# Kernel tuning notes

Measured on AMD Instinct MI355X. Metric: run time of the kernel, lower is better.

Reference implementation:

```python
import jax, jax.numpy as jnp
import numpy as np

B = 32        # num graphs
N = 512       # nodes per graph (equal-sized blocks)
HID = 512     # hidden_dim
H = 8         # num_heads
E = 262144    # num edges
ED = 16       # edge feature dim


def setup_inputs() -> dict:
    key = jax.random.key(0)
    ks = jax.random.split(key, 12)
    x = jax.random.normal(ks[0], (B * N, HID), jnp.float32)
    # contiguous, sorted graph assignment (equal-sized graphs)
    batch = jnp.repeat(jnp.arange(B, dtype=jnp.int64), N)
    # within-graph random edges
    g = jax.random.randint(ks[1], (E,), 0, B)
    src = g * N + jax.random.randint(ks[2], (E,), 0, N)
    dst = g * N + jax.random.randint(ks[3], (E,), 0, N)
    edge_index = jnp.stack([src, dst]).astype(jnp.int64)
    edge_attr = jax.random.normal(ks[4], (E, ED), jnp.float32)
    s = 1.0 / np.sqrt(HID).astype(np.float32)
    Wq = jax.random.normal(ks[5], (HID, HID), jnp.float32) * s
    Wk = jax.random.normal(ks[6], (HID, HID), jnp.float32) * s
    Wv = jax.random.normal(ks[7], (HID, HID), jnp.float32) * s
    Wo = jax.random.normal(ks[8], (HID, HID), jnp.float32) * s
    We = jax.random.normal(ks[9], (ED, H), jnp.float32) * (1.0 / np.sqrt(ED).astype(np.float32))
    bq = jnp.zeros((HID,), jnp.float32)
    bk = jnp.zeros((HID,), jnp.float32)
    bv = jnp.zeros((HID,), jnp.float32)
    bo = jnp.zeros((HID,), jnp.float32)
    be = jnp.zeros((H,), jnp.float32)
    return dict(x=x, batch=batch, edge_index=edge_index, edge_attr=edge_attr,
                Wq=Wq, bq=bq, Wk=Wk, bk=bk, Wv=Wv, bv=bv, Wo=Wo, bo=bo,
                We=We, be=be, num_graphs=B)


def reference(x, batch, edge_index, edge_attr, Wq, bq, Wk, bk, Wv, bv, Wo, bo, We, be, num_graphs):
    n_total, hid = x.shape
    n = n_total // num_graphs           # nodes per graph (equal blocks)
    hd = hid // H                       # head_dim
    scale = 1.0 / jnp.sqrt(jnp.asarray(hd, x.dtype))
    q = (x @ Wq + bq).reshape(num_graphs, n, H, hd)
    k = (x @ Wk + bk).reshape(num_graphs, n, H, hd)
    v = (x @ Wv + bv).reshape(num_graphs, n, H, hd)
    # per-graph dense scores: [B, n(query), m(key), H]
    attn = jnp.einsum('bnhd,bmhd->bnmh', q, k) * scale
    # edge-bias scatter-add (edges are intra-graph; local coords via div/mod)
    eb = edge_attr @ We + be                      # [E, H]
    b_idx = edge_index[0] // n
    loc_src = edge_index[0] % n
    loc_dst = edge_index[1] % n
    attn = attn.at[b_idx, loc_src, loc_dst].add(eb)
    # softmax over key axis (torch dim=1 of 'nmh' == axis 2 here)
    attn = jax.nn.softmax(attn, axis=2)
    out = jnp.einsum('bnmh,bmhd->bnhd', attn, v).reshape(n_total, hid)
    return out @ Wo + bo
```

## Files before the change

kernel.cpp:

```cpp
#include <hip/hip_runtime.h>
#include <stdint.h>

typedef unsigned short u16;
typedef __bf16 bf16x8 __attribute__((ext_vector_type(8)));
typedef short  short8 __attribute__((ext_vector_type(8)));
typedef float  f32x4  __attribute__((ext_vector_type(4)));
typedef float  float4v __attribute__((ext_vector_type(4)));
typedef uint32_t u32x2 __attribute__((ext_vector_type(2)));

#define NG    32
#define NPG   512
#define HIDD  512
#define NH    8
#define HD    64
#define NE    262144
#define NNODE (NG*NPG)

__device__ __forceinline__ float fexp2(float x) { return __builtin_amdgcn_exp2f(x); }

__device__ __forceinline__ u16 f2bf(float f) {
  union { float f; uint32_t u; } x; x.f = f;
  uint32_t r = x.u + 0x7FFFu + ((x.u >> 16) & 1u);
  return (u16)(r >> 16);
}
__device__ __forceinline__ float bf2f(u16 b) {
  union { uint32_t u; float f; } x; x.u = ((uint32_t)b) << 16;
  return x.f;
}
__device__ __forceinline__ uint32_t pkbf(float a, float b) {
  __bf16 x = (__bf16)a, y = (__bf16)b;
  return (uint32_t)__builtin_bit_cast(u16, x) | ((uint32_t)__builtin_bit_cast(u16, y) << 16);
}
__device__ __forceinline__ bf16x8 ldfrag(const u16* p) {
  short8 t = *(const short8*)p;
  return __builtin_bit_cast(bf16x8, t);
}
__device__ __forceinline__ f32x4 mfma16(bf16x8 a, bf16x8 b, f32x4 c) {
  return __builtin_amdgcn_mfma_f32_16x16x32_bf16(a, b, c, 0, 0, 0);
}
__device__ __forceinline__ void gl2lds16(const void* g, void* l) {
  __builtin_amdgcn_global_load_lds((const __attribute__((address_space(1))) void*)g,
                                   (__attribute__((address_space(3))) void*)l, 16, 0, 0);
}
__device__ __forceinline__ void st(u16* p, float v)   { *p = f2bf(v); }
__device__ __forceinline__ void st(float* p, float v) { *p = v; }


__global__ void k_cast_x(const float* __restrict__ x, u16* __restrict__ xb) {
  size_t i = ((size_t)blockIdx.x * 256 + threadIdx.x) * 8;
  float4v v0 = *(const float4v*)(x + i);
  float4v v1 = *(const float4v*)(x + i + 4);
  short8 r;
  r[0]=(short)f2bf(v0[0]); r[1]=(short)f2bf(v0[1]); r[2]=(short)f2bf(v0[2]); r[3]=(short)f2bf(v0[3]);
  r[4]=(short)f2bf(v1[0]); r[5]=(short)f2bf(v1[1]); r[6]=(short)f2bf(v1[2]); r[7]=(short)f2bf(v1[3]);
  *(short8*)(xb + i) = r;
}

__global__ void k_transw(const float* __restrict__ W0, const float* __restrict__ W1,
                         const float* __restrict__ W2, const float* __restrict__ W3,
                         u16* __restrict__ wt) {
  const float* W = blockIdx.z==0 ? W0 : blockIdx.z==1 ? W1 : blockIdx.z==2 ? W2 : W3;
  u16* out = wt + (size_t)blockIdx.z * HIDD * HIDD;
  __shared__ float tl[32][33];
  int tx = threadIdx.x, ty = threadIdx.y;
  int x0 = blockIdx.x * 32, y0 = blockIdx.y * 32;
  #pragma unroll
  for (int i = 0; i < 4; ++i) tl[ty + i*8][tx] = W[(size_t)(y0 + ty + i*8) * HIDD + x0 + tx];
  __syncthreads();
  #pragma unroll
  for (int i = 0; i < 4; ++i) out[(size_t)(x0 + ty + i*8) * HIDD + (y0 + tx)] = f2bf(tl[tx][ty + i*8]);
}

__global__ void k_count2(const int* __restrict__ ei, int* __restrict__ counts) {
  int e = blockIdx.x * 256 + threadIdx.x;
  int src = ei[e];
  int dl  = ei[NE + e] & (NPG - 1);
  atomicAdd(&counts[src * 8 + (dl >> 6)], 1);
}

__global__ void k_scan_a(const int* __restrict__ counts, int* __restrict__ rowstart,
                         int* __restrict__ bsum) {
  __shared__ int arr[256];
  int t = threadIdx.x;
  int i = blockIdx.x * 256 + t;
  int c = counts[i];
  arr[t] = c;
  __syncthreads();
  for (int off = 1; off < 256; off <<= 1) {
    int v = (t >= off) ? arr[t - off] : 0;
    __syncthreads();
    arr[t] += v;
    __syncthreads();
  }
  rowstart[i] = arr[t] - c;
  if (t == 255) bsum[blockIdx.x] = arr[255];
}
__global__ void k_scan_b(int* __restrict__ bsum) {
  __shared__ int arr[512];
  int t = threadIdx.x;
  int c = bsum[t];
  arr[t] = c;
  __syncthreads();
  for (int off = 1; off < 512; off <<= 1) {
    int v = (t >= off) ? arr[t - off] : 0;
    __syncthreads();
    arr[t] += v;
    __syncthreads();
  }
  bsum[t] = arr[t] - c;
}
__global__ void k_scan_c(const int* __restrict__ bsum, int* __restrict__ rowstart) {
  int i = blockIdx.x * 256 + threadIdx.x;
  rowstart[i] += bsum[blockIdx.x];
  if (i == 0) rowstart[131072] = NE;
}

__global__ void k_fill(const int* __restrict__ ei, const float* __restrict__ ea,
                       const float* __restrict__ We, const float* __restrict__ be,
                       const int* __restrict__ rowstart, int* __restrict__ cursor,
                       uint32_t* __restrict__ packed) {
  __shared__ float w[128];
  __shared__ float bb[8];
  int t = threadIdx.x;
  if (t < 128) w[t] = We[t];
  if (t < 8)   bb[t] = be[t];
  __syncthreads();
  int e = blockIdx.x * 256 + t;
  int src = ei[e];
  int dl  = ei[NE + e] & (NPG - 1);
  const float* ap = ea + (size_t)e * 16;
  float a[16];
  #pragma unroll
  for (int i = 0; i < 16; i += 4) {
    float4v v = *(const float4v*)(ap + i);
    a[i]=v[0]; a[i+1]=v[1]; a[i+2]=v[2]; a[i+3]=v[3];
  }
  float acc[8];
  #pragma unroll
  for (int hh = 0; hh < 8; ++hh) acc[hh] = bb[hh];
  #pragma unroll
  for (int d = 0; d < 16; ++d)
    #pragma unroll
    for (int hh = 0; hh < 8; ++hh) acc[hh] += a[d] * w[d*8 + hh];
  int bin = src * 8 + (dl >> 6);
  int pos = atomicAdd(&cursor[bin], 1);
  size_t base = ((size_t)(rowstart[bin] + pos)) * 8;
  #pragma unroll
  for (int hh = 0; hh < 8; ++hh) {
    float m = fexp2(acc[hh] * 1.44269504089f);
    union { _Float16 hf; u16 us; } cv; cv.hf = (_Float16)m;
    packed[base + hh] = (uint32_t)(dl & 63) | ((uint32_t)cv.us << 16);
  }
}


template <typename OT, bool VOUT>
__device__ void gemm_body(u16* smem, const u16* __restrict__ A, const u16* __restrict__ Bt,
                          const float* __restrict__ bias, OT* __restrict__ C,
                          u16* __restrict__ vtg, float oscale) {
  const int tid = threadIdx.x;
  const int w = tid >> 6, l = tid & 63, lr = l & 15, lg = l >> 4;
  const int idl = blockIdx.x + (blockIdx.y << 2);
  const int nid = (idl & 7) * 64 + (idl >> 3);
  const int bn0 = (nid & 3) * 128, bm0 = (nid >> 2) * 128;
  const int wr = w >> 1, wc = w & 1;
  f32x4 acc[4][4];
  #pragma unroll
  for (int i = 0; i < 4; ++i)
    #pragma unroll
    for (int j = 0; j < 4; ++j) acc[i][j] = (f32x4){0.f, 0.f, 0.f, 0.f};

  const int o1 = w * 1024 + l * 16;
  auto stageAB = [&](int kt, int buf) {
    #pragma unroll
    for (int rnd = 0; rnd < 2; ++rnd) {
      const int o = rnd * 4096 + o1;
      const int row = o >> 6, colb = o & 63;
      gl2lds16((const char*)A  + ((size_t)(bm0 + row) * HIDD + kt * 32) * 2 + colb,
               (char*)smem + buf * 8192 + o);
      gl2lds16((const char*)Bt + ((size_t)(bn0 + row) * HIDD + kt * 32) * 2 + colb,
               (char*)smem + 16384 + buf * 8192 + o);
    }
  };

  stageAB(0, 0);
  for (int kt = 0; kt < 16; ++kt) {
    if (kt < 15) {
      stageAB(kt + 1, (kt + 1) & 1);
      asm volatile("s_waitcnt vmcnt(4)" ::: "memory");
    } else {
      asm volatile("s_waitcnt vmcnt(0)" ::: "memory");
    }
    __syncthreads();
    const u16* Ab = smem + (kt & 1) * 4096;
    const u16* Bb = smem + 8192 + (kt & 1) * 4096;
    bf16x8 af[4], bfr[4];
    #pragma unroll
    for (int i = 0; i < 4; ++i) af[i]  = ldfrag(&Ab[(wr*64 + i*16 + lr) * 32 + lg*8]);
    #pragma unroll
    for (int j = 0; j < 4; ++j) bfr[j] = ldfrag(&Bb[(wc*64 + j*16 + lr) * 32 + lg*8]);
    #pragma unroll
    for (int i = 0; i < 4; ++i)
      #pragma unroll
      for (int j = 0; j < 4; ++j)
        acc[i][j] = mfma16(af[i], bfr[j], acc[i][j]);
    __syncthreads();
  }

  if constexpr (VOUT) {
    #pragma unroll
    for (int j = 0; j < 4; ++j) {
      const int d = j * 16 + lr;
      const float bv = bias[bn0 + wc*64 + j*16 + lr];
      #pragma unroll
      for (int i = 0; i < 4; ++i) {
        const int t4 = wc * 2 + wr;
        const int byteo = t4 * 8192 + d * 128 + ((i*32 + lg*8) ^ ((d & 7) << 4));
        uint32_t lo = pkbf(acc[i][j][0] + bv, acc[i][j][1] + bv);
        uint32_t hi = pkbf(acc[i][j][2] + bv, acc[i][j][3] + bv);
        *(u32x2*)((char*)smem + byteo) = (u32x2){lo, hi};
      }
    }
    __syncthreads();
    const int b = bm0 >> 9, kt0 = (bm0 & 511) >> 6, h0 = bn0 >> 6;
    #pragma unroll
    for (int t4 = 0; t4 < 4; ++t4) {
      size_t base = ((size_t)(b * 8 + h0 + (t4 >> 1)) * 8 + kt0 + (t4 & 1)) * 4096;
      #pragma unroll
      for (int rnd = 0; rnd < 2; ++rnd) {
        int idx = rnd * 256 + tid;
        *(short8*)(vtg + base + idx * 8) = *(const short8*)&smem[t4 * 4096 + idx * 8];
      }
    }
  } else {
    #pragma unroll
    for (int j = 0; j < 4; ++j) {
      const int col = bn0 + wc*64 + j*16 + lr;
      const float bv = bias[col];
      #pragma unroll
      for (int i = 0; i < 4; ++i) {
        const int row0 = bm0 + wr*64 + i*16 + lg*4;
        #pragma unroll
        for (int q = 0; q < 4; ++q)
          st(&C[(size_t)(row0 + q) * HIDD + col], (acc[i][j][q] + bv) * oscale);
      }
    }
  }
}

__global__ __launch_bounds__(256, 3) void k_gemm_qkv(
    const u16* __restrict__ A, const u16* __restrict__ Wt,
    const float* __restrict__ b0, const float* __restrict__ b1, const float* __restrict__ b2,
    u16* __restrict__ O0, u16* __restrict__ O1, u16* __restrict__ vtg) {
  __shared__ u16 smem[16384];
  const float c1 = 0.125f * 1.44269504089f;
  int z = blockIdx.z;
  const u16* Bt = Wt + (size_t)z * HIDD * HIDD;
  if (z == 0)      gemm_body<u16, false>(smem, A, Bt, b0, O0, nullptr, c1);
  else if (z == 1) gemm_body<u16, false>(smem, A, Bt, b1, O1, nullptr, 1.0f);
  else             gemm_body<u16, true >(smem, A, Bt, b2, nullptr, vtg, 1.0f);
}

__global__ __launch_bounds__(256, 3) void k_gemm_out(
    const u16* __restrict__ A, const u16* __restrict__ Bt,
    const float* __restrict__ bias, float* __restrict__ C) {
  __shared__ u16 smem[16384];
  gemm_body<float, false>(smem, A, Bt, bias, C, nullptr, 1.0f);
}


__global__ __launch_bounds__(256, 4) void k_attn(
    const u16* __restrict__ qb, const u16* __restrict__ kb, const u16* __restrict__ vtg,
    const uint32_t* __restrict__ packed, const int* __restrict__ rowstart2,
    u16* __restrict__ ab) {
  __shared__ u16 kl[4096];
  __shared__ u16 vl[4096];
  __shared__ u16 pl[4][2048];
  const int tid = threadIdx.x, w = tid >> 6, l = tid & 63, lr = l & 15, lg = l >> 4;

  const int id = blockIdx.x;
  const int nid = (id & 7) * 128 + (id >> 3);
  const int q0 = (nid & 3) * 128;
  const int h  = (nid >> 2) & 7;
  const int b  = nid >> 5;
  const int bh = b * 8 + h;
  const int rbase = q0 + w * 32;
  u16* plw = &pl[w][0];
  const int pswz = (lr & 7) << 4;

  bf16x8 qf[2][2];
  #pragma unroll
  for (int g = 0; g < 2; ++g) {
    const u16* qp = qb + (size_t)(b * NPG + rbase + g * 16 + lr) * HIDD + h * HD + lg * 8;
    qf[g][0] = ldfrag(qp);
    qf[g][1] = ldfrag(qp + 32);
  }

  auto stageK = [&](int kt) {
    #pragma unroll
    for (int rnd = 0; rnd < 2; ++rnd) {
      int o = rnd * 4096 + w * 1024 + l * 16;
      int key = o >> 7, db = o & 127;
      int col = db ^ ((key & 7) << 4);
      gl2lds16((const char*)kb + ((size_t)(b * NPG + kt * 64 + key) * HIDD + h * HD) * 2 + col,
               (char*)kl + o);
    }
  };
  auto stageV = [&](int kt) {
    #pragma unroll
    for (int rnd = 0; rnd < 2; ++rnd) {
      int o = rnd * 4096 + w * 1024 + l * 16;
      gl2lds16((const char*)vtg + ((size_t)(bh * 8 + kt)) * 8192 + o,
               (char*)vl + o);
    }
  };

  float rs[2] = {0.f, 0.f};
  f32x4 oacc[2][4];
  #pragma unroll
  for (int g = 0; g < 2; ++g)
    #pragma unroll
    for (int dt = 0; dt < 4; ++dt) oacc[g][dt] = (f32x4){0.f, 0.f, 0.f, 0.f};

  stageK(0); stageV(0);

  const int ge = lg & 1, ecls = lg >> 1;
  const int egrow = b * NPG + rbase + ge * 16 + lr;
  int eA = rowstart2[egrow * 8];
  int eB = rowstart2[egrow * 8 + 1];

  for (int kt = 0; kt < 8; ++kt) {
    asm volatile("s_waitcnt vmcnt(0)" ::: "memory");
    __syncthreads();

    int eC = (kt < 7) ? rowstart2[egrow * 8 + kt + 2] : 0;
    int s0c = (eA < eB) ? eA : 0;
    uint32_t u0 = packed[(size_t)s0c * 8 + h];

    f32x4 s4[2][4];
    __builtin_amdgcn_s_setprio(1);
    #pragma unroll
    for (int sub = 0; sub < 4; ++sub) {
      int key = sub * 16 + lr;
      bf16x8 kf0, kf1;
      {
        int db0 = ((lg * 8) * 2) ^ ((key & 7) << 4);
        int db1 = ((32 + lg * 8) * 2) ^ ((key & 7) << 4);
        kf0 = ldfrag(&kl[(key * 128 + db0) >> 1]);
        kf1 = ldfrag(&kl[(key * 128 + db1) >> 1]);
      }
      #pragma unroll
      for (int g = 0; g < 2; ++g) {
        s4[g][sub] = mfma16(kf0, qf[g][0], (f32x4){0.f, 0.f, 0.f, 0.f});
        s4[g][sub] = mfma16(kf1, qf[g][1], s4[g][sub]);
      }
    }
    __builtin_amdgcn_s_setprio(0);

    #pragma unroll
    for (int g = 0; g < 2; ++g) {
      const int prow = g * 16 + lr;
      #pragma unroll
      for (int sub = 0; sub < 4; ++sub) {
        float p0 = fexp2(s4[g][sub][0]);
        float p1 = fexp2(s4[g][sub][1]);
        float p2 = fexp2(s4[g][sub][2]);
        float p3 = fexp2(s4[g][sub][3]);
        rs[g] += (p0 + p1) + (p2 + p3);
        uint32_t lo = pkbf(p0, p1);
        uint32_t hi = pkbf(p2, p3);
        *(u32x2*)((char*)plw + prow * 128 + ((sub * 32 + lg * 8) ^ pswz)) = (u32x2){lo, hi};
      }
    }
    asm volatile("s_waitcnt lgkmcnt(0)" ::: "memory");
    __builtin_amdgcn_sched_barrier(0);

    {
      float delta = 0.f;
      const int re = ge * 16 + lr;
      uint32_t u = u0;
      for (int s = eA; s < eB; ++s) {
        uint32_t ucur = u;
        if (s + 1 < eB) u = packed[(size_t)(s + 1) * 8 + h];
        int dl = (int)(ucur & 63u);
        if ((dl & 1) == ecls) {
          union { u16 us; _Float16 hf; } cv; cv.us = (u16)(ucur >> 16);
          float mult = (float)cv.hf;
          int idx = (re * 128 + ((dl * 2) ^ pswz)) >> 1;
          float old = bf2f(plw[idx]);
          plw[idx] = f2bf(old * mult);
          delta += old * (mult - 1.0f);
        }
      }
      rs[0] += (ge == 0) ? delta : 0.f;
      rs[1] += (ge == 1) ? delta : 0.f;
    }
    asm volatile("s_waitcnt lgkmcnt(0)" ::: "memory");
    __builtin_amdgcn_sched_barrier(0);

    __builtin_amdgcn_s_setprio(1);
    #pragma unroll
    for (int ks = 0; ks < 2; ++ks) {
      bf16x8 pa0 = ldfrag(&plw[(lr * 128 + ((ks * 64 + lg * 16) ^ pswz)) >> 1]);
      bf16x8 pa1 = ldfrag(&plw[((16 + lr) * 128 + ((ks * 64 + lg * 16) ^ pswz)) >> 1]);
      #pragma unroll
      for (int dt = 0; dt < 4; ++dt) {
        int d = dt * 16 + lr;
        bf16x8 vf = ldfrag(&vl[(d * 128 + ((ks * 64 + lg * 16) ^ ((d & 7) << 4))) >> 1]);
        oacc[0][dt] = mfma16(vf, pa0, oacc[0][dt]);
        oacc[1][dt] = mfma16(vf, pa1, oacc[1][dt]);
      }
    }
    __builtin_amdgcn_s_setprio(0);

    __syncthreads();
    if (kt < 7) { stageK(kt + 1); stageV(kt + 1); }
    eA = eB; eB = eC;
  }

  #pragma unroll
  for (int g = 0; g < 2; ++g) {
    float tot = rs[g] + __shfl_xor(rs[g], 16, 64);
    tot += __shfl_xor(tot, 32, 64);
    float inv = 1.0f / tot;
    const size_t grow = (size_t)(b * NPG + rbase + g * 16 + lr);
    #pragma unroll
    for (int dt = 0; dt < 4; ++dt) {
      uint32_t lo = pkbf(oacc[g][dt][0] * inv, oacc[g][dt][1] * inv);
      uint32_t hi = pkbf(oacc[g][dt][2] * inv, oacc[g][dt][3] * inv);
      *(u32x2*)(ab + grow * HIDD + h * HD + dt * 16 + lg * 4) = (u32x2){lo, hi};
    }
  }
}


extern "C" void kernel_launch(void* const* d_in, const int* in_sizes, int n_in,
                              void* d_out, int out_size, void* d_ws, size_t ws_size,
                              hipStream_t stream) {
  const float* x  = (const float*)d_in[0];
  const int*   ei = (const int*)d_in[2];
  const float* ea = (const float*)d_in[3];
  const float* Wq = (const float*)d_in[4];  const float* bq = (const float*)d_in[5];
  const float* Wk = (const float*)d_in[6];  const float* bk = (const float*)d_in[7];
  const float* Wv = (const float*)d_in[8];  const float* bv = (const float*)d_in[9];
  const float* Wo = (const float*)d_in[10]; const float* bo = (const float*)d_in[11];
  const float* We = (const float*)d_in[12]; const float* be = (const float*)d_in[13];

  char* ws = (char*)d_ws;
  const size_t MB = 1 << 20;
  u16*  xb  = (u16*)(ws);
  u16*  wt  = (u16*)(ws + 16*MB);
  u16*  qbp = (u16*)(ws + 18*MB);
  u16*  kbp = (u16*)(ws + 34*MB);
  u16*  vtg = (u16*)(ws + 50*MB);
  uint32_t* packed = (uint32_t*)(ws + 66*MB);
  int*  rowstart2 = (int*)(ws + 74*MB);
  int*  bsum      = (int*)(ws + 74*MB + 640*1024);
  int*  counts2  = (int*)(ws + 50*MB);
  int*  cursor2  = (int*)(ws + 50*MB + 512*1024);
  u16*  ab = xb;

  (void)hipMemsetAsync(counts2, 0, 2 * 512 * 1024, stream);

  k_cast_x<<<dim3(NNODE * HIDD / (256 * 8)), 256, 0, stream>>>(x, xb);
  k_transw<<<dim3(16, 16, 4), dim3(32, 8, 1), 0, stream>>>(Wq, Wk, Wv, Wo, wt);
  k_count2<<<dim3(NE / 256), 256, 0, stream>>>(ei, counts2);
  k_scan_a<<<dim3(512), 256, 0, stream>>>(counts2, rowstart2, bsum);
  k_scan_b<<<dim3(1), 512, 0, stream>>>(bsum);
  k_scan_c<<<dim3(512), 256, 0, stream>>>(bsum, rowstart2);
  k_fill<<<dim3(NE / 256), 256, 0, stream>>>(ei, ea, We, be, rowstart2, cursor2, packed);

  k_gemm_qkv<<<dim3(HIDD / 128, NNODE / 128, 3), 256, 0, stream>>>(
      xb, wt, bq, bk, bv, qbp, kbp, vtg);

  k_attn<<<dim3(1024), 256, 0, stream>>>(qbp, kbp, vtg, packed, rowstart2, ab);

  k_gemm_out<<<dim3(HIDD / 128, NNODE / 128, 1), 256, 0, stream>>>(
      ab, wt + (size_t)3 * HIDD * HIDD, bo, (float*)d_out);
}
```

Baseline: 161.2 us.

## Merge prep kernels and replace three-pass scan with atomic-offset scan

Folds the x cast, weight transpose and edge counting into one launch, indexed by block id. The three-kernel prefix scan is replaced by a single kernel in which each block claims a base offset with a global atomic, so bucket order is no longer the global order. Because of that, explicit row-end arrays are written, and the attention kernel reads start/end pairs instead of consecutive starts. This cuts four launches, at the cost of non-deterministic bucket placement and an extra row-end load per tile.

```diff
diff --git a/kernel.cpp b/kernel.cpp
--- a/kernel.cpp
+++ b/kernel.cpp
@@ -46,44 +46,49 @@
 __device__ __forceinline__ void st(float* p, float v) { *p = v; }
 
 
-__global__ void k_cast_x(const float* __restrict__ x, u16* __restrict__ xb) {
-  size_t i = ((size_t)blockIdx.x * 256 + threadIdx.x) * 8;
-  float4v v0 = *(const float4v*)(x + i);
-  float4v v1 = *(const float4v*)(x + i + 4);
-  short8 r;
-  r[0]=(short)f2bf(v0[0]); r[1]=(short)f2bf(v0[1]); r[2]=(short)f2bf(v0[2]); r[3]=(short)f2bf(v0[3]);
-  r[4]=(short)f2bf(v1[0]); r[5]=(short)f2bf(v1[1]); r[6]=(short)f2bf(v1[2]); r[7]=(short)f2bf(v1[3]);
-  *(short8*)(xb + i) = r;
-}
-
-__global__ void k_transw(const float* __restrict__ W0, const float* __restrict__ W1,
-                         const float* __restrict__ W2, const float* __restrict__ W3,
-                         u16* __restrict__ wt) {
-  const float* W = blockIdx.z==0 ? W0 : blockIdx.z==1 ? W1 : blockIdx.z==2 ? W2 : W3;
-  u16* out = wt + (size_t)blockIdx.z * HIDD * HIDD;
+__global__ void k_prep(const float* __restrict__ x, u16* __restrict__ xb,
+                       const float* __restrict__ W0, const float* __restrict__ W1,
+                       const float* __restrict__ W2, const float* __restrict__ W3,
+                       u16* __restrict__ wt,
+                       const int* __restrict__ ei, int* __restrict__ counts) {
   __shared__ float tl[32][33];
-  int tx = threadIdx.x, ty = threadIdx.y;
-  int x0 = blockIdx.x * 32, y0 = blockIdx.y * 32;
-  #pragma unroll
-  for (int i = 0; i < 4; ++i) tl[ty + i*8][tx] = W[(size_t)(y0 + ty + i*8) * HIDD + x0 + tx];
-  __syncthreads();
-  #pragma unroll
-  for (int i = 0; i < 4; ++i) out[(size_t)(x0 + ty + i*8) * HIDD + (y0 + tx)] = f2bf(tl[tx][ty + i*8]);
-}
-
-__global__ void k_count2(const int* __restrict__ ei, int* __restrict__ counts) {
-  int e = blockIdx.x * 256 + threadIdx.x;
-  int src = ei[e];
-  int dl  = ei[NE + e] & (NPG - 1);
-  atomicAdd(&counts[src * 8 + (dl >> 6)], 1);
-}
-
-__global__ void k_scan_a(const int* __restrict__ counts, int* __restrict__ rowstart,
-                         int* __restrict__ bsum) {
+  const int bid = blockIdx.x, t = threadIdx.x;
+  if (bid < 4096) {
+    size_t i = ((size_t)bid * 256 + t) * 8;
+    float4v v0 = *(const float4v*)(x + i);
+    float4v v1 = *(const float4v*)(x + i + 4);
+    short8 r;
+    r[0]=(short)f2bf(v0[0]); r[1]=(short)f2bf(v0[1]); r[2]=(short)f2bf(v0[2]); r[3]=(short)f2bf(v0[3]);
+    r[4]=(short)f2bf(v1[0]); r[5]=(short)f2bf(v1[1]); r[6]=(short)f2bf(v1[2]); r[7]=(short)f2bf(v1[3]);
+    *(short8*)(xb + i) = r;
+  } else if (bid < 5120) {
+    const int id2 = bid - 4096;
+    const int z = id2 >> 8, rem = id2 & 255;
+    const int y0 = (rem >> 4) * 32, x0 = (rem & 15) * 32;
+    const float* W = z==0 ? W0 : z==1 ? W1 : z==2 ? W2 : W3;
+    u16* out = wt + (size_t)z * HIDD * HIDD;
+    const int tx = t & 31, ty = t >> 5;
+    #pragma unroll
+    for (int i = 0; i < 4; ++i) tl[ty + i*8][tx] = W[(size_t)(y0 + ty + i*8) * HIDD + x0 + tx];
+    __syncthreads();
+    #pragma unroll
+    for (int i = 0; i < 4; ++i) out[(size_t)(x0 + ty + i*8) * HIDD + (y0 + tx)] = f2bf(tl[tx][ty + i*8]);
+  } else {
+    int e = (bid - 5120) * 256 + t;
+    int src = ei[e];
+    int dl  = ei[NE + e] & (NPG - 1);
+    atomicAdd(&counts[src * 8 + (dl >> 6)], 1);
+  }
+}
+
+
+__global__ void k_scan_u(const int* __restrict__ counts, int* __restrict__ rowstart,
+                         int* __restrict__ rowend, int* __restrict__ gcur) {
   __shared__ int arr[256];
-  int t = threadIdx.x;
-  int i = blockIdx.x * 256 + t;
-  int c = counts[i];
+  __shared__ int basesh;
+  const int t = threadIdx.x;
+  const int i = blockIdx.x * 256 + t;
+  const int c = counts[i];
   arr[t] = c;
   __syncthreads();
   for (int off = 1; off < 256; off <<= 1) {
@@ -92,27 +97,12 @@
     arr[t] += v;
     __syncthreads();
   }
-  rowstart[i] = arr[t] - c;
-  if (t == 255) bsum[blockIdx.x] = arr[255];
-}
-__global__ void k_scan_b(int* __restrict__ bsum) {
-  __shared__ int arr[512];
-  int t = threadIdx.x;
-  int c = bsum[t];
-  arr[t] = c;
+  const int incl = arr[t];
+  if (t == 255) basesh = atomicAdd(gcur, incl);
   __syncthreads();
-  for (int off = 1; off < 512; off <<= 1) {
-    int v = (t >= off) ? arr[t - off] : 0;
-    __syncthreads();
-    arr[t] += v;
-    __syncthreads();
-  }
-  bsum[t] = arr[t] - c;
-}
-__global__ void k_scan_c(const int* __restrict__ bsum, int* __restrict__ rowstart) {
-  int i = blockIdx.x * 256 + threadIdx.x;
-  rowstart[i] += bsum[blockIdx.x];
-  if (i == 0) rowstart[131072] = NE;
+  const int base = basesh;
+  rowstart[i] = base + incl - c;
+  rowend[i]   = base + incl;
 }
 
 __global__ void k_fill(const int* __restrict__ ei, const float* __restrict__ ea,
@@ -272,7 +262,7 @@
 __global__ __launch_bounds__(256, 4) void k_attn(
     const u16* __restrict__ qb, const u16* __restrict__ kb, const u16* __restrict__ vtg,
     const uint32_t* __restrict__ packed, const int* __restrict__ rowstart2,
-    u16* __restrict__ ab) {
+    const int* __restrict__ rowend2, u16* __restrict__ ab) {
   __shared__ u16 kl[4096];
   __shared__ u16 vl[4096];
   __shared__ u16 pl[4][2048];
@@ -327,14 +317,15 @@
   const int ge = lg & 1, ecls = lg >> 1;
   const int egrow = b * NPG + rbase + ge * 16 + lr;
   int eA = rowstart2[egrow * 8];
-  int eB = rowstart2[egrow * 8 + 1];
+  int eE = rowend2[egrow * 8];
 
   for (int kt = 0; kt < 8; ++kt) {
     asm volatile("s_waitcnt vmcnt(0)" ::: "memory");
     __syncthreads();
 
-    int eC = (kt < 7) ? rowstart2[egrow * 8 + kt + 2] : 0;
-    int s0c = (eA < eB) ? eA : 0;
+    int sN = (kt < 7) ? rowstart2[egrow * 8 + kt + 1] : 0;
+    int eN = (kt < 7) ? rowend2[egrow * 8 + kt + 1] : 0;
+    int s0c = (eA < eE) ? eA : 0;
     uint32_t u0 = packed[(size_t)s0c * 8 + h];
 
     f32x4 s4[2][4];
@@ -379,9 +370,9 @@
       float delta = 0.f;
       const int re = ge * 16 + lr;
       uint32_t u = u0;
-      for (int s = eA; s < eB; ++s) {
+      for (int s = eA; s < eE; ++s) {
         uint32_t ucur = u;
-        if (s + 1 < eB) u = packed[(size_t)(s + 1) * 8 + h];
+        if (s + 1 < eE) u = packed[(size_t)(s + 1) * 8 + h];
         int dl = (int)(ucur & 63u);
         if ((dl & 1) == ecls) {
           union { u16 us; _Float16 hf; } cv; cv.us = (u16)(ucur >> 16);
@@ -415,7 +406,7 @@
 
     __syncthreads();
     if (kt < 7) { stageK(kt + 1); stageV(kt + 1); }
-    eA = eB; eB = eC;
+    eA = sN; eE = eN;
   }
 
   #pragma unroll
@@ -455,25 +446,22 @@
   u16*  vtg = (u16*)(ws + 50*MB);
   uint32_t* packed = (uint32_t*)(ws + 66*MB);
   int*  rowstart2 = (int*)(ws + 74*MB);
-  int*  bsum      = (int*)(ws + 74*MB + 640*1024);
+  int*  rowend2   = (int*)(ws + 74*MB + 640*1024);
   int*  counts2  = (int*)(ws + 50*MB);
   int*  cursor2  = (int*)(ws + 50*MB + 512*1024);
+  int*  gcur     = (int*)(ws + 51*MB);
   u16*  ab = xb;
 
-  (void)hipMemsetAsync(counts2, 0, 2 * 512 * 1024, stream);
-
-  k_cast_x<<<dim3(NNODE * HIDD / (256 * 8)), 256, 0, stream>>>(x, xb);
-  k_transw<<<dim3(16, 16, 4), dim3(32, 8, 1), 0, stream>>>(Wq, Wk, Wv, Wo, wt);
-  k_count2<<<dim3(NE / 256), 256, 0, stream>>>(ei, counts2);
-  k_scan_a<<<dim3(512), 256, 0, stream>>>(counts2, rowstart2, bsum);
-  k_scan_b<<<dim3(1), 512, 0, stream>>>(bsum);
-  k_scan_c<<<dim3(512), 256, 0, stream>>>(bsum, rowstart2);
+  (void)hipMemsetAsync(counts2, 0, 1024 * 1024 + 64, stream);
+
+  k_prep<<<dim3(6144), 256, 0, stream>>>(x, xb, Wq, Wk, Wv, Wo, wt, ei, counts2);
+  k_scan_u<<<dim3(512), 256, 0, stream>>>(counts2, rowstart2, rowend2, gcur);
   k_fill<<<dim3(NE / 256), 256, 0, stream>>>(ei, ea, We, be, rowstart2, cursor2, packed);
 
   k_gemm_qkv<<<dim3(HIDD / 128, NNODE / 128, 3), 256, 0, stream>>>(
       xb, wt, bq, bk, bv, qbp, kbp, vtg);
 
-  k_attn<<<dim3(1024), 256, 0, stream>>>(qbp, kbp, vtg, packed, rowstart2, ab);
+  k_attn<<<dim3(1024), 256, 0, stream>>>(qbp, kbp, vtg, packed, rowstart2, rowend2, ab);
 
   k_gemm_out<<<dim3(HIDD / 128, NNODE / 128, 1), 256, 0, stream>>>(
       ab, wt + (size_t)3 * HIDD * HIDD, bo, (float*)d_out);
```

New measurement: 159.3 us, median of 2. About the same (-1.2%).
